# Performance work log

Measured on AMD Instinct MI355X. Metric: run time of the kernel, lower is better.

The kernel has to match this reference:

```python
import jax, jax.numpy as jnp
import numpy as np

DIM = 512
HEADS = 16
HD = DIM // HEADS            # head_dim = 32
WH, WW = 8, 8                # window_size
D0, D1 = 2, 2                # dilated_size
TWH, TWW = WH * D0, WW * D1  # total_window_size = 16,16
SCALE = HD ** -0.5


def _wpart(x, wh, ww):
    # (B,H,W,C) -> (B * H/wh * W/ww, wh, ww, C)
    B, H, W, C = x.shape
    x = x.reshape(B, H // wh, wh, W // ww, ww, C)
    return x.transpose(0, 1, 3, 2, 4, 5).reshape(-1, wh, ww, C)


def _wrev(win, wh, ww, H, W):
    # (nW*B, wh, ww, C) -> (B, H, W, C)
    C = win.shape[-1]
    B = win.shape[0] // ((H // wh) * (W // ww))
    x = win.reshape(B, H // wh, W // ww, wh, ww, C).transpose(0, 1, 3, 2, 4, 5)
    return x.reshape(B, H, W, C)


def _rope2(x):
    # 2D RoPE over a (B, WH, WW, HD) window: first half of HD rotated by row
    # position, second half by column position (axial rotary embedding).
    d = HD // 2
    inv = 1.0 / (10000.0 ** (jnp.arange(0, d, 2, dtype=jnp.float32) / d))  # (d/2,)

    def rot(xp, ang):
        x1, x2 = xp[..., 0::2], xp[..., 1::2]
        c, s = jnp.cos(ang), jnp.sin(ang)
        return jnp.stack([x1 * c - x2 * s, x1 * s + x2 * c], axis=-1).reshape(xp.shape)

    ah = (jnp.arange(WH, dtype=jnp.float32)[:, None] * inv)[:, None, :]  # (WH,1,d/2)
    aw = (jnp.arange(WW, dtype=jnp.float32)[:, None] * inv)[None, :, :]  # (1,WW,d/2)
    return jnp.concatenate([rot(x[..., :d], ah), rot(x[..., d:], aw)], axis=-1)


def _forward(x, qkv_w, qkv_b, proj_w, proj_b):
    B, H, W, C = x.shape
    # partition into total windows, then dilated regrouping
    xw = _wpart(x, TWH, TWW)                                   # (B_, 16, 16, C)
    B_ = xw.shape[0]
    xw = _wpart(xw, D0, D1)                                    # (B_*64, 2, 2, C)
    xw = xw.reshape(B_, WH * WW, D0 * D1, C)
    xw = xw.transpose(0, 2, 1, 3).reshape(B_ * D0 * D1, WH * WW, C)  # (B__, N, C)
    B__, N = xw.shape[0], xw.shape[1]

    qkv = (xw @ qkv_w.T + qkv_b).reshape(B__, N, 3, HEADS, HD).transpose(2, 0, 3, 1, 4)
    q, k, v = qkv[0], qkv[1], qkv[2]                           # (B__, HEADS, N, HD)

    q = _rope2(q.reshape(-1, WH, WW, HD)).reshape(B__, HEADS, N, HD) * SCALE
    k = _rope2(k.reshape(-1, WH, WW, HD)).reshape(B__, HEADS, N, HD)

    attn = jax.nn.softmax(jnp.einsum('bhnd,bhmd->bhnm', q, k), axis=-1)
    out = jnp.einsum('bhnm,bhmd->bhnd', attn, v)               # (B__, HEADS, N, HD)
    out = out.transpose(0, 2, 1, 3).reshape(B__, N, C)

    # undo dilated regrouping, then undo total-window partition
    out = out.reshape(B_, D0 * D1, N, C).transpose(0, 2, 1, 3).reshape(-1, D0, D1, C)
    out = _wrev(out, D0, D1, TWH, TWW)                         # (B_, 16, 16, C)
    out = _wrev(out, TWH, TWW, H, W)                           # (B, H, W, C)
    return out @ proj_w.T + proj_b


def setup_inputs() -> dict:
    key = jax.random.key(0)
    k0, k1, k2 = jax.random.split(key, 3)
    x = jax.random.normal(k0, (4, 128, 128, DIM), dtype=jnp.float32)
    qkv_w = jax.random.normal(k1, (3 * DIM, DIM), dtype=jnp.float32) * (DIM ** -0.5)
    qkv_b = jnp.zeros((3 * DIM,), dtype=jnp.float32)
    proj_w = jax.random.normal(k2, (DIM, DIM), dtype=jnp.float32) * (DIM ** -0.5)
    proj_b = jnp.zeros((DIM,), dtype=jnp.float32)
    return {"x": x, "qkv_w": qkv_w, "qkv_b": qkv_b, "proj_w": proj_w, "proj_b": proj_b}


def reference(x, qkv_w, qkv_b, proj_w, proj_b):
    return _forward(x, qkv_w, qkv_b, proj_w, proj_b)
```

## Files before the change

### kernel.cpp

```cpp
#include <hip/hip_runtime.h>
#include <hip/hip_bf16.h>
#include <stdint.h>

#define DIMC  512
#define NHEAD 16
#define HDIM  32
#define NTOK  65536
#define QKVN  1536
static constexpr float SCALE_F = 0.17677669529663687f;

typedef __attribute__((ext_vector_type(4))) float  f32x4;
typedef __attribute__((ext_vector_type(8))) __bf16 bf16x8;

__device__ __forceinline__ uint16_t f2bf(float f) {
  union { float f; uint32_t u; } v; v.f = f;
  return (uint16_t)((v.u + 0x7FFFu + ((v.u >> 16) & 1u)) >> 16);
}

__device__ __forceinline__ void gload_lds16(const void* g, void* l) {
  __builtin_amdgcn_global_load_lds((const __attribute__((address_space(1))) void*)g,
                                   (__attribute__((address_space(3))) void*)l,
                                   16, 0, 0);
}

__global__ void cvt_f32_bf16(const float* __restrict__ src,
                             uint16_t* __restrict__ dst, int n4)
{
  int i = blockIdx.x * blockDim.x + threadIdx.x;
  const int stride = gridDim.x * blockDim.x;
  for (; i < n4; i += stride) {
    const float4 v = ((const float4*)src)[i];
    ushort4 o;
    o.x = f2bf(v.x); o.y = f2bf(v.y); o.z = f2bf(v.z); o.w = f2bf(v.w);
    ((ushort4*)dst)[i] = o;
  }
}

template <bool OUT_F32>
__global__ __launch_bounds__(512, 2)
void gemm256_8ph(const uint16_t* __restrict__ A,
                 const uint16_t* __restrict__ B,
                 const float* __restrict__ bias,
                 void* __restrict__ Cv,
                 int M, int N, int K, int gx)
{
  __shared__ __align__(16) char lds[131072];

  const int tid = threadIdx.x;
  const int l  = tid & 63, w = tid >> 6;
  const int wm = w >> 2,  wn = w & 3;
  const int lm = l & 15,  lq = l >> 4;

  const int nwg = gridDim.x;
  const int qq = nwg >> 3, rr = nwg & 7;
  const int xcd = blockIdx.x & 7, loc = blockIdx.x >> 3;
  const int sw = (xcd < rr ? xcd * (qq + 1) : rr * (qq + 1) + (xcd - rr) * qq) + loc;
  const long m0 = (long)(sw / gx) * 256;
  const long n0 = (long)(sw % gx) * 256;

  const int srow  = tid >> 3;
  const int scolb = (((tid & 7) ^ (srow & 7)) << 4);
  const uint16_t* Ags = A + (m0 + srow) * (long)K + (scolb >> 1);
  const uint16_t* Bgs = B + (n0 + srow) * (long)K + (scolb >> 1);
  char* ldsW = lds + (w << 10);

#define STAGE(Gs, regionOff, half, kt)                                        \
  {                                                                           \
    const uint16_t* s0_ = (Gs) + (size_t)((half) * 128) * K + (kt);           \
    gload_lds16(s0_,                  ldsW + (regionOff));                    \
    gload_lds16(s0_ + (size_t)64 * K, ldsW + (regionOff) + 8192);             \
  }

  const int colx0 = ((lq ^ (lm & 7)) << 4);
  const int aoff0 = (wm * 64 + lm) * 128 + colx0;
  const int aoff1 = (wm * 64 + lm) * 128 + (colx0 ^ 64);
  const int boff0 = (wn * 32 + lm) * 128 + colx0;
  const int boff1 = (wn * 32 + lm) * 128 + (colx0 ^ 64);

  f32x4  acc[2][2][4][2] = {};
  bf16x8 aX[4][2], aY[4][2];
  bf16x8 b0[2][2], b1[2][2];

#define RD_A(DST, OFF)                                                        \
  _Pragma("unroll") for (int i = 0; i < 4; ++i) {                             \
    DST[i][0] = *(const bf16x8*)(lds + (OFF) + aoff0 + i * 2048);             \
    DST[i][1] = *(const bf16x8*)(lds + (OFF) + aoff1 + i * 2048);             \
  }
#define RD_B(DST, OFF)                                                        \
  _Pragma("unroll") for (int j = 0; j < 2; ++j) {                             \
    DST[j][0] = *(const bf16x8*)(lds + (OFF) + boff0 + j * 2048);             \
    DST[j][1] = *(const bf16x8*)(lds + (OFF) + boff1 + j * 2048);             \
  }
#define MFMA16(AS, BS, QM, QN)                                                \
  __builtin_amdgcn_s_setprio(1);                                              \
  _Pragma("unroll") for (int kk = 0; kk < 2; ++kk)                            \
    _Pragma("unroll") for (int i = 0; i < 4; ++i)                             \
      _Pragma("unroll") for (int j = 0; j < 2; ++j)                           \
        acc[QM][QN][i][j] = __builtin_amdgcn_mfma_f32_16x16x32_bf16(          \
            AS[i][kk], BS[j][kk], acc[QM][QN][i][j], 0, 0, 0);                \
  __builtin_amdgcn_s_setprio(0);
#define VMW(N) asm volatile("s_waitcnt vmcnt(" #N ")");
#define BAR()  __builtin_amdgcn_s_barrier();

  STAGE(Ags, 0,             0, 0)
  STAGE(Bgs, 32768,         0, 0)
  STAGE(Ags, 16384,         1, 0)
  STAGE(Bgs, 49152,         1, 0)
  STAGE(Ags, 65536,         0, 64)
  STAGE(Bgs, 65536 + 32768, 0, 64)
  VMW(8) BAR()
  RD_A(aX, 0) RD_B(b0, 32768)
  VMW(4) BAR()

  for (int t2 = 0; t2 < K / 64; t2 += 2) {
    const int k1 = (t2 + 1) * 64;
    int k2 = (t2 + 2) * 64; if (k2 >= K) k2 = 0;
    int k3 = (t2 + 3) * 64; if (k3 >= K) k3 = 0;

    RD_B(b1, 49152)                 STAGE(Ags, 65536 + 16384, 1, k1)
    MFMA16(aX, b0, 0, 0)            BAR()
    RD_A(aY, 16384)                 STAGE(Bgs, 65536 + 49152, 1, k1)
    MFMA16(aX, b1, 0, 1)            BAR()
    STAGE(Ags, 0, 0, k2)
    MFMA16(aY, b0, 1, 0)            VMW(6) BAR()
    RD_A(aX, 65536) RD_B(b0, 65536 + 32768)
    STAGE(Bgs, 32768, 0, k2)
    MFMA16(aY, b1, 1, 1)            VMW(4) BAR()
    RD_B(b1, 65536 + 49152)         STAGE(Ags, 16384, 1, k2)
    MFMA16(aX, b0, 0, 0)            BAR()
    RD_A(aY, 65536 + 16384)         STAGE(Bgs, 49152, 1, k2)
    MFMA16(aX, b1, 0, 1)            BAR()
    STAGE(Ags, 65536, 0, k3)
    MFMA16(aY, b0, 1, 0)            VMW(6) BAR()
    RD_A(aX, 0) RD_B(b0, 32768)
    STAGE(Bgs, 65536 + 32768, 0, k3)
    MFMA16(aY, b1, 1, 1)            VMW(4) BAR()
  }
#undef STAGE
#undef RD_A
#undef RD_B
#undef MFMA16
#undef VMW
#undef BAR

#pragma unroll
  for (int qm = 0; qm < 2; ++qm)
#pragma unroll
  for (int qn = 0; qn < 2; ++qn)
#pragma unroll
  for (int i = 0; i < 4; ++i)
#pragma unroll
  for (int j = 0; j < 2; ++j) {
    const long m = m0 + qm * 128 + wm * 64 + i * 16 + lq * 4;
    const long n = n0 + qn * 128 + wn * 32 + j * 16 + lm;
    const float bv = bias[n];
#pragma unroll
    for (int r = 0; r < 4; ++r) {
      const float val = acc[qm][qn][i][j][r] + bv;
      if (OUT_F32) ((float*)Cv)[(m + r) * (long)N + n] = val;
      else         ((uint16_t*)Cv)[(m + r) * (long)N + n] = f2bf(val);
    }
  }
}

__global__ void attn_win(const uint16_t* __restrict__ QKV,
                         uint16_t* __restrict__ O)
{
  __shared__ __align__(16) __bf16 Pl[4][64][72];

  const int tid = threadIdx.x;
  const int l  = tid & 63, w = tid >> 6;
  const int lm = l & 15,  lq = l >> 4;
  const int bid = blockIdx.x;
  const int g = bid >> 2;
  const int h = (bid & 3) * 4 + w;

  const int d1 = g & 1, d0 = (g >> 1) & 1;
  const int wx = (g >> 2) & 7, wy = (g >> 5) & 7, bb = g >> 8;
  const long tbase = ((long)(bb * 128 + wy * 16 + d0) * 128) + wx * 16 + d1;

  f32x4 invs;
#pragma unroll
  for (int i = 0; i < 4; ++i)
    invs[i] = exp2f(-1.6609640474436813f * (float)((lq & 1) * 4 + i));

  const int co_q = h * HDIM;
  const int co_k = DIMC + h * HDIM;
  const int co_v = 2 * DIMC + h * HDIM;

  bf16x8 qf[4], kf[4];
#pragma unroll
  for (int f = 0; f < 4; ++f) {
    const int n  = f * 16 + lm;
    const int iy = n >> 3, ix = n & 7;
    const float pos = (lq < 2) ? (float)iy : (float)ix;
    const long t = tbase + iy * 256 + ix * 2;
    const uint16_t* qp = QKV + t * QKVN + co_q + lq * 8;
    const uint16_t* kp = QKV + t * QKVN + co_k + lq * 8;
    {
      bf16x8 raw = *(const bf16x8*)qp, o;
#pragma unroll
      for (int i = 0; i < 4; ++i) {
        float x1 = (float)raw[2 * i], x2 = (float)raw[2 * i + 1];
        float s, c; __sincosf(pos * invs[i], &s, &c);
        o[2 * i]     = (__bf16)((x1 * c - x2 * s) * SCALE_F);
        o[2 * i + 1] = (__bf16)((x1 * s + x2 * c) * SCALE_F);
      }
      qf[f] = o;
    }
    {
      bf16x8 raw = *(const bf16x8*)kp, o;
#pragma unroll
      for (int i = 0; i < 4; ++i) {
        float x1 = (float)raw[2 * i], x2 = (float)raw[2 * i + 1];
        float s, c; __sincosf(pos * invs[i], &s, &c);
        o[2 * i]     = (__bf16)(x1 * c - x2 * s);
        o[2 * i + 1] = (__bf16)(x1 * s + x2 * c);
      }
      kf[f] = o;
    }
  }

  const f32x4 fzero = {0.f, 0.f, 0.f, 0.f};
  f32x4 s[4][4];
#pragma unroll
  for (int mi = 0; mi < 4; ++mi)
#pragma unroll
    for (int ni = 0; ni < 4; ++ni)
      s[mi][ni] = __builtin_amdgcn_mfma_f32_16x16x32_bf16(qf[mi], kf[ni], fzero, 0, 0, 0);

  float rsum[4][4];
#pragma unroll
  for (int mi = 0; mi < 4; ++mi)
#pragma unroll
    for (int r = 0; r < 4; ++r) {
      float m = s[mi][0][r];
#pragma unroll
      for (int ni = 1; ni < 4; ++ni) m = fmaxf(m, s[mi][ni][r]);
      m = fmaxf(m, __shfl_xor(m, 1));
      m = fmaxf(m, __shfl_xor(m, 2));
      m = fmaxf(m, __shfl_xor(m, 4));
      m = fmaxf(m, __shfl_xor(m, 8));
      float sum = 0.f;
#pragma unroll
      for (int ni = 0; ni < 4; ++ni) {
        float p = expf(s[mi][ni][r] - m);
        s[mi][ni][r] = p;
        sum += p;
      }
      sum += __shfl_xor(sum, 1);
      sum += __shfl_xor(sum, 2);
      sum += __shfl_xor(sum, 4);
      sum += __shfl_xor(sum, 8);
      rsum[mi][r] = sum;
    }

#pragma unroll
  for (int mi = 0; mi < 4; ++mi)
#pragma unroll
    for (int ni = 0; ni < 4; ++ni)
#pragma unroll
      for (int r = 0; r < 4; ++r)
        Pl[w][mi * 16 + lq * 4 + r][ni * 16 + lm] = (__bf16)s[mi][ni][r];

  bf16x8 pa[4][2];
#pragma unroll
  for (int mi = 0; mi < 4; ++mi)
#pragma unroll
    for (int kk = 0; kk < 2; ++kk)
      pa[mi][kk] = *(const bf16x8*)(&Pl[w][mi * 16 + lm][kk * 32 + lq * 8]);

  bf16x8 vf[2][2];
#pragma unroll
  for (int kk = 0; kk < 2; ++kk)
#pragma unroll
    for (int n2 = 0; n2 < 2; ++n2) {
      const int nb = kk * 32 + lq * 8;
      const long tb2 = tbase + (long)(nb >> 3) * 256;
      const uint16_t* vp = QKV + co_v + n2 * 16 + lm;
      bf16x8 o;
#pragma unroll
      for (int i = 0; i < 8; ++i)
        o[i] = *(const __bf16*)(vp + (tb2 + 2 * i) * QKVN);
      vf[kk][n2] = o;
    }

  f32x4 oacc[4][2] = {};
#pragma unroll
  for (int kk = 0; kk < 2; ++kk)
#pragma unroll
    for (int mi = 0; mi < 4; ++mi)
#pragma unroll
      for (int n2 = 0; n2 < 2; ++n2)
        oacc[mi][n2] = __builtin_amdgcn_mfma_f32_16x16x32_bf16(
            pa[mi][kk], vf[kk][n2], oacc[mi][n2], 0, 0, 0);

#pragma unroll
  for (int mi = 0; mi < 4; ++mi)
#pragma unroll
    for (int r = 0; r < 4; ++r) {
      const int n = mi * 16 + lq * 4 + r;
      const long t = tbase + (n >> 3) * 256 + (n & 7) * 2;
      const float rinv = 1.0f / rsum[mi][r];
#pragma unroll
      for (int n2 = 0; n2 < 2; ++n2)
        O[t * DIMC + h * HDIM + n2 * 16 + lm] = f2bf(oacc[mi][n2][r] * rinv);
    }
}

extern "C" void kernel_launch(void* const* d_in, const int* in_sizes, int n_in,
                              void* d_out, int out_size, void* d_ws, size_t ws_size,
                              hipStream_t stream)
{
  const float* x      = (const float*)d_in[0];
  const float* qkv_w  = (const float*)d_in[1];
  const float* qkv_b  = (const float*)d_in[2];
  const float* proj_w = (const float*)d_in[3];
  const float* proj_b = (const float*)d_in[4];
  float* out = (float*)d_out;

  uint16_t* xb    = (uint16_t*)d_ws;
  uint16_t* qwb   = xb    + (size_t)NTOK * DIMC;
  uint16_t* pwb   = qwb   + (size_t)QKVN * DIMC;
  uint16_t* qkv   = pwb   + (size_t)DIMC * DIMC;
  uint16_t* attn  = qkv   + (size_t)NTOK * QKVN;

  cvt_f32_bf16<<<2048, 256, 0, stream>>>(x,      xb,  NTOK * DIMC / 4);
  cvt_f32_bf16<<<512,  256, 0, stream>>>(qkv_w,  qwb, QKVN * DIMC / 4);
  cvt_f32_bf16<<<256,  256, 0, stream>>>(proj_w, pwb, DIMC * DIMC / 4);

  gemm256_8ph<false><<<dim3((NTOK / 256) * (QKVN / 256)), dim3(512), 0, stream>>>(
      xb, qwb, qkv_b, qkv, NTOK, QKVN, DIMC, QKVN / 256);

  attn_win<<<dim3(1024 * 4), dim3(256), 0, stream>>>(qkv, attn);

  gemm256_8ph<true><<<dim3((NTOK / 256) * (DIMC / 256)), dim3(512), 0, stream>>>(
      attn, pwb, proj_b, out, NTOK, DIMC, DIMC, DIMC / 256);
}
```

Measured before the change: 297.2 us.

## Fuse QKV projection with windowed attention in one kernel per window

```diff
diff --git a/kernel.cpp b/kernel.cpp
--- a/kernel.cpp
+++ b/kernel.cpp
@@ -33,6 +33,200 @@
     ushort4 o;
     o.x = f2bf(v.x); o.y = f2bf(v.y); o.z = f2bf(v.z); o.w = f2bf(v.w);
     ((ushort4*)dst)[i] = o;
+  }
+}
+
+__global__ __launch_bounds__(512, 1)
+void fused_qkv_attn(const float* __restrict__ x,
+                    const uint16_t* __restrict__ Wq,
+                    const float* __restrict__ qkv_b,
+                    uint16_t* __restrict__ O)
+{
+  __shared__ __align__(16) __bf16 xs[64][512];
+  __shared__ __align__(16) __bf16 scr[8][64][72];
+
+  const int tid = threadIdx.x;
+  const int l  = tid & 63, w = tid >> 6;
+  const int lm = l & 15,  lq = l >> 4;
+  const int g = blockIdx.x;
+  const int d1 = g & 1, d0 = (g >> 1) & 1;
+  const int wx = (g >> 2) & 7, wy = (g >> 5) & 7, bb = g >> 8;
+  const long tbase = ((long)(bb * 128 + wy * 16 + d0) * 128) + wx * 16 + d1;
+
+  char* xsC = (char*)&xs[0][0];
+
+#pragma unroll
+  for (int pass = 0; pass < 8; ++pass) {
+    const int G = pass * 512 + tid;
+    const int row = G >> 6, u = G & 63;
+    const long t = tbase + (row >> 3) * 256 + (row & 7) * 2;
+    const float* src = x + t * DIMC + u * 8;
+    const f32x4 v0 = *(const f32x4*)src;
+    const f32x4 v1 = *(const f32x4*)(src + 4);
+    bf16x8 o;
+#pragma unroll
+    for (int q = 0; q < 4; ++q) { o[q] = (__bf16)v0[q]; o[q + 4] = (__bf16)v1[q]; }
+    *(bf16x8*)(xsC + row * 1024 + ((u ^ (row & 7)) << 4)) = o;
+  }
+  __syncthreads();
+
+  __bf16 (*Sw)[72] = scr[w];
+
+  f32x4 invs;
+#pragma unroll
+  for (int i = 0; i < 4; ++i)
+    invs[i] = exp2f(-1.6609640474436813f * (float)((lq & 1) * 4 + i));
+
+  const f32x4 fzero = {0.f, 0.f, 0.f, 0.f};
+
+  auto gemm_to_scr = [&](int wrow0) {
+    f32x4 acc[4][2] = {};
+    const uint16_t* Wp = Wq + (size_t)wrow0 * DIMC;
+#pragma unroll
+    for (int st = 0; st < 16; ++st) {
+      bf16x8 b[2], a[4];
+#pragma unroll
+      for (int j = 0; j < 2; ++j)
+        b[j] = *(const bf16x8*)(Wp + (size_t)(j * 16 + lm) * DIMC + st * 32 + lq * 8);
+#pragma unroll
+      for (int i = 0; i < 4; ++i)
+        a[i] = *(const bf16x8*)(xsC + (i * 16 + lm) * 1024 +
+                                (((st * 4 + lq) ^ (lm & 7)) << 4));
+#pragma unroll
+      for (int i = 0; i < 4; ++i)
+#pragma unroll
+        for (int j = 0; j < 2; ++j)
+          acc[i][j] = __builtin_amdgcn_mfma_f32_16x16x32_bf16(
+              a[i], b[j], acc[i][j], 0, 0, 0);
+    }
+    const float b0 = qkv_b[wrow0 + lm];
+    const float b1 = qkv_b[wrow0 + 16 + lm];
+#pragma unroll
+    for (int mi = 0; mi < 4; ++mi)
+#pragma unroll
+      for (int r = 0; r < 4; ++r) {
+        Sw[mi * 16 + lq * 4 + r][lm]      = (__bf16)(acc[mi][0][r] + b0);
+        Sw[mi * 16 + lq * 4 + r][16 + lm] = (__bf16)(acc[mi][1][r] + b1);
+      }
+  };
+
+  for (int hp = 0; hp < 2; ++hp) {
+    const int h = w * 2 + hp;
+
+    gemm_to_scr(h * HDIM);
+    bf16x8 qf[4], kf[4];
+#pragma unroll
+    for (int f = 0; f < 4; ++f) {
+      const int n = f * 16 + lm, iy = n >> 3, ix = n & 7;
+      const float pos = (lq < 2) ? (float)iy : (float)ix;
+      bf16x8 raw = *(const bf16x8*)&Sw[n][lq * 8], o;
+#pragma unroll
+      for (int i = 0; i < 4; ++i) {
+        float x1 = (float)raw[2 * i], x2 = (float)raw[2 * i + 1];
+        float s_, c_; __sincosf(pos * invs[i], &s_, &c_);
+        o[2 * i]     = (__bf16)((x1 * c_ - x2 * s_) * SCALE_F);
+        o[2 * i + 1] = (__bf16)((x1 * s_ + x2 * c_) * SCALE_F);
+      }
+      qf[f] = o;
+    }
+    gemm_to_scr(DIMC + h * HDIM);
+#pragma unroll
+    for (int f = 0; f < 4; ++f) {
+      const int n = f * 16 + lm, iy = n >> 3, ix = n & 7;
+      const float pos = (lq < 2) ? (float)iy : (float)ix;
+      bf16x8 raw = *(const bf16x8*)&Sw[n][lq * 8], o;
+#pragma unroll
+      for (int i = 0; i < 4; ++i) {
+        float x1 = (float)raw[2 * i], x2 = (float)raw[2 * i + 1];
+        float s_, c_; __sincosf(pos * invs[i], &s_, &c_);
+        o[2 * i]     = (__bf16)(x1 * c_ - x2 * s_);
+        o[2 * i + 1] = (__bf16)(x1 * s_ + x2 * c_);
+      }
+      kf[f] = o;
+    }
+    gemm_to_scr(2 * DIMC + h * HDIM);
+    bf16x8 vf[2][2];
+#pragma unroll
+    for (int kk = 0; kk < 2; ++kk)
+#pragma unroll
+      for (int n2 = 0; n2 < 2; ++n2) {
+        bf16x8 o;
+#pragma unroll
+        for (int i = 0; i < 8; ++i)
+          o[i] = Sw[kk * 32 + lq * 8 + i][n2 * 16 + lm];
+        vf[kk][n2] = o;
+      }
+
+    f32x4 s[4][4];
+#pragma unroll
+    for (int mi = 0; mi < 4; ++mi)
+#pragma unroll
+      for (int ni = 0; ni < 4; ++ni)
+        s[mi][ni] = __builtin_amdgcn_mfma_f32_16x16x32_bf16(
+            qf[mi], kf[ni], fzero, 0, 0, 0);
+
+    float rsum[4][4];
+#pragma unroll
+    for (int mi = 0; mi < 4; ++mi)
+#pragma unroll
+      for (int r = 0; r < 4; ++r) {
+        float m = s[mi][0][r];
+#pragma unroll
+        for (int ni = 1; ni < 4; ++ni) m = fmaxf(m, s[mi][ni][r]);
+        m = fmaxf(m, __shfl_xor(m, 1));
+        m = fmaxf(m, __shfl_xor(m, 2));
+        m = fmaxf(m, __shfl_xor(m, 4));
+        m = fmaxf(m, __shfl_xor(m, 8));
+        float sum = 0.f;
+#pragma unroll
+        for (int ni = 0; ni < 4; ++ni) {
+          float p = expf(s[mi][ni][r] - m);
+          s[mi][ni][r] = p;
+          sum += p;
+        }
+        sum += __shfl_xor(sum, 1);
+        sum += __shfl_xor(sum, 2);
+        sum += __shfl_xor(sum, 4);
+        sum += __shfl_xor(sum, 8);
+        rsum[mi][r] = sum;
+      }
+
+#pragma unroll
+    for (int mi = 0; mi < 4; ++mi)
+#pragma unroll
+      for (int ni = 0; ni < 4; ++ni)
+#pragma unroll
+        for (int r = 0; r < 4; ++r)
+          Sw[mi * 16 + lq * 4 + r][ni * 16 + lm] = (__bf16)s[mi][ni][r];
+
+    bf16x8 pa[4][2];
+#pragma unroll
+    for (int mi = 0; mi < 4; ++mi)
+#pragma unroll
+      for (int kk = 0; kk < 2; ++kk)
+        pa[mi][kk] = *(const bf16x8*)(&Sw[mi * 16 + lm][kk * 32 + lq * 8]);
+
+    f32x4 oacc[4][2] = {};
+#pragma unroll
+    for (int kk = 0; kk < 2; ++kk)
+#pragma unroll
+      for (int mi = 0; mi < 4; ++mi)
+#pragma unroll
+        for (int n2 = 0; n2 < 2; ++n2)
+          oacc[mi][n2] = __builtin_amdgcn_mfma_f32_16x16x32_bf16(
+              pa[mi][kk], vf[kk][n2], oacc[mi][n2], 0, 0, 0);
+
+#pragma unroll
+    for (int mi = 0; mi < 4; ++mi)
+#pragma unroll
+      for (int r = 0; r < 4; ++r) {
+        const int n = mi * 16 + lq * 4 + r;
+        const long t = tbase + (n >> 3) * 256 + (n & 7) * 2;
+        const float rinv = 1.0f / rsum[mi][r];
+#pragma unroll
+        for (int n2 = 0; n2 < 2; ++n2)
+          O[t * DIMC + h * HDIM + n2 * 16 + lm] = f2bf(oacc[mi][n2][r] * rinv);
+      }
   }
 }
 
@@ -163,151 +357,6 @@
   }
 }
 
-__global__ void attn_win(const uint16_t* __restrict__ QKV,
-                         uint16_t* __restrict__ O)
-{
-  __shared__ __align__(16) __bf16 Pl[4][64][72];
-
-  const int tid = threadIdx.x;
-  const int l  = tid & 63, w = tid >> 6;
-  const int lm = l & 15,  lq = l >> 4;
-  const int bid = blockIdx.x;
-  const int g = bid >> 2;
-  const int h = (bid & 3) * 4 + w;
-
-  const int d1 = g & 1, d0 = (g >> 1) & 1;
-  const int wx = (g >> 2) & 7, wy = (g >> 5) & 7, bb = g >> 8;
-  const long tbase = ((long)(bb * 128 + wy * 16 + d0) * 128) + wx * 16 + d1;
-
-  f32x4 invs;
-#pragma unroll
-  for (int i = 0; i < 4; ++i)
-    invs[i] = exp2f(-1.6609640474436813f * (float)((lq & 1) * 4 + i));
-
-  const int co_q = h * HDIM;
-  const int co_k = DIMC + h * HDIM;
-  const int co_v = 2 * DIMC + h * HDIM;
-
-  bf16x8 qf[4], kf[4];
-#pragma unroll
-  for (int f = 0; f < 4; ++f) {
-    const int n  = f * 16 + lm;
-    const int iy = n >> 3, ix = n & 7;
-    const float pos = (lq < 2) ? (float)iy : (float)ix;
-    const long t = tbase + iy * 256 + ix * 2;
-    const uint16_t* qp = QKV + t * QKVN + co_q + lq * 8;
-    const uint16_t* kp = QKV + t * QKVN + co_k + lq * 8;
-    {
-      bf16x8 raw = *(const bf16x8*)qp, o;
-#pragma unroll
-      for (int i = 0; i < 4; ++i) {
-        float x1 = (float)raw[2 * i], x2 = (float)raw[2 * i + 1];
-        float s, c; __sincosf(pos * invs[i], &s, &c);
-        o[2 * i]     = (__bf16)((x1 * c - x2 * s) * SCALE_F);
-        o[2 * i + 1] = (__bf16)((x1 * s + x2 * c) * SCALE_F);
-      }
-      qf[f] = o;
-    }
-    {
-      bf16x8 raw = *(const bf16x8*)kp, o;
-#pragma unroll
-      for (int i = 0; i < 4; ++i) {
-        float x1 = (float)raw[2 * i], x2 = (float)raw[2 * i + 1];
-        float s, c; __sincosf(pos * invs[i], &s, &c);
-        o[2 * i]     = (__bf16)(x1 * c - x2 * s);
-        o[2 * i + 1] = (__bf16)(x1 * s + x2 * c);
-      }
-      kf[f] = o;
-    }
-  }
-
-  const f32x4 fzero = {0.f, 0.f, 0.f, 0.f};
-  f32x4 s[4][4];
-#pragma unroll
-  for (int mi = 0; mi < 4; ++mi)
-#pragma unroll
-    for (int ni = 0; ni < 4; ++ni)
-      s[mi][ni] = __builtin_amdgcn_mfma_f32_16x16x32_bf16(qf[mi], kf[ni], fzero, 0, 0, 0);
-
-  float rsum[4][4];
-#pragma unroll
-  for (int mi = 0; mi < 4; ++mi)
-#pragma unroll
-    for (int r = 0; r < 4; ++r) {
-      float m = s[mi][0][r];
-#pragma unroll
-      for (int ni = 1; ni < 4; ++ni) m = fmaxf(m, s[mi][ni][r]);
-      m = fmaxf(m, __shfl_xor(m, 1));
-      m = fmaxf(m, __shfl_xor(m, 2));
-      m = fmaxf(m, __shfl_xor(m, 4));
-      m = fmaxf(m, __shfl_xor(m, 8));
-      float sum = 0.f;
-#pragma unroll
-      for (int ni = 0; ni < 4; ++ni) {
-        float p = expf(s[mi][ni][r] - m);
-        s[mi][ni][r] = p;
-        sum += p;
-      }
-      sum += __shfl_xor(sum, 1);
-      sum += __shfl_xor(sum, 2);
-      sum += __shfl_xor(sum, 4);
-      sum += __shfl_xor(sum, 8);
-      rsum[mi][r] = sum;
-    }
-
-#pragma unroll
-  for (int mi = 0; mi < 4; ++mi)
-#pragma unroll
-    for (int ni = 0; ni < 4; ++ni)
-#pragma unroll
-      for (int r = 0; r < 4; ++r)
-        Pl[w][mi * 16 + lq * 4 + r][ni * 16 + lm] = (__bf16)s[mi][ni][r];
-
-  bf16x8 pa[4][2];
-#pragma unroll
-  for (int mi = 0; mi < 4; ++mi)
-#pragma unroll
-    for (int kk = 0; kk < 2; ++kk)
-      pa[mi][kk] = *(const bf16x8*)(&Pl[w][mi * 16 + lm][kk * 32 + lq * 8]);
-
-  bf16x8 vf[2][2];
-#pragma unroll
-  for (int kk = 0; kk < 2; ++kk)
-#pragma unroll
-    for (int n2 = 0; n2 < 2; ++n2) {
-      const int nb = kk * 32 + lq * 8;
-      const long tb2 = tbase + (long)(nb >> 3) * 256;
-      const uint16_t* vp = QKV + co_v + n2 * 16 + lm;
-      bf16x8 o;
-#pragma unroll
-      for (int i = 0; i < 8; ++i)
-        o[i] = *(const __bf16*)(vp + (tb2 + 2 * i) * QKVN);
-      vf[kk][n2] = o;
-    }
-
-  f32x4 oacc[4][2] = {};
-#pragma unroll
-  for (int kk = 0; kk < 2; ++kk)
-#pragma unroll
-    for (int mi = 0; mi < 4; ++mi)
-#pragma unroll
-      for (int n2 = 0; n2 < 2; ++n2)
-        oacc[mi][n2] = __builtin_amdgcn_mfma_f32_16x16x32_bf16(
-            pa[mi][kk], vf[kk][n2], oacc[mi][n2], 0, 0, 0);
-
-#pragma unroll
-  for (int mi = 0; mi < 4; ++mi)
-#pragma unroll
-    for (int r = 0; r < 4; ++r) {
-      const int n = mi * 16 + lq * 4 + r;
-      const long t = tbase + (n >> 3) * 256 + (n & 7) * 2;
-      const float rinv = 1.0f / rsum[mi][r];
-#pragma unroll
-      for (int n2 = 0; n2 < 2; ++n2)
-        O[t * DIMC + h * HDIM + n2 * 16 + lm] = f2bf(oacc[mi][n2][r] * rinv);
-    }
-}
-
 extern "C" void kernel_launch(void* const* d_in, const int* in_sizes, int n_in,
                               void* d_out, int out_size, void* d_ws, size_t ws_size,
                               hipStream_t stream)
@@ -319,20 +368,14 @@
   const float* proj_b = (const float*)d_in[4];
   float* out = (float*)d_out;
 
-  uint16_t* xb    = (uint16_t*)d_ws;
-  uint16_t* qwb   = xb    + (size_t)NTOK * DIMC;
-  uint16_t* pwb   = qwb   + (size_t)QKVN * DIMC;
-  uint16_t* qkv   = pwb   + (size_t)DIMC * DIMC;
-  uint16_t* attn  = qkv   + (size_t)NTOK * QKVN;
-
-  cvt_f32_bf16<<<2048, 256, 0, stream>>>(x,      xb,  NTOK * DIMC / 4);
-  cvt_f32_bf16<<<512,  256, 0, stream>>>(qkv_w,  qwb, QKVN * DIMC / 4);
-  cvt_f32_bf16<<<256,  256, 0, stream>>>(proj_w, pwb, DIMC * DIMC / 4);
-
-  gemm256_8ph<false><<<dim3((NTOK / 256) * (QKVN / 256)), dim3(512), 0, stream>>>(
-      xb, qwb, qkv_b, qkv, NTOK, QKVN, DIMC, QKVN / 256);
-
-  attn_win<<<dim3(1024 * 4), dim3(256), 0, stream>>>(qkv, attn);
+  uint16_t* qwb  = (uint16_t*)d_ws;
+  uint16_t* pwb  = qwb + (size_t)QKVN * DIMC;
+  uint16_t* attn = pwb + (size_t)DIMC * DIMC;
+
+  cvt_f32_bf16<<<512, 256, 0, stream>>>(qkv_w,  qwb, QKVN * DIMC / 4);
+  cvt_f32_bf16<<<256, 256, 0, stream>>>(proj_w, pwb, DIMC * DIMC / 4);
+
+  fused_qkv_attn<<<dim3(1024), dim3(512), 0, stream>>>(x, qwb, qkv_b, attn);
 
   gemm256_8ph<true><<<dim3((NTOK / 256) * (DIMC / 256)), dim3(512), 0, stream>>>(
       attn, pwb, proj_b, out, NTOK, DIMC, DIMC, DIMC / 256);
```

New measurement: 399.6 us. 1.34x slower.

## Fuse windowed attention with output projection GEMM in one kernel

Applied to the files above, without the earlier changes.

```diff
diff --git a/kernel.cpp b/kernel.cpp
--- a/kernel.cpp
+++ b/kernel.cpp
@@ -163,148 +163,209 @@
   }
 }
 
-__global__ void attn_win(const uint16_t* __restrict__ QKV,
-                         uint16_t* __restrict__ O)
+__global__ __launch_bounds__(512, 2)
+void attn_proj(const uint16_t* __restrict__ QKV,
+               const uint16_t* __restrict__ Wp,
+               const float* __restrict__ proj_b,
+               float* __restrict__ out)
 {
-  __shared__ __align__(16) __bf16 Pl[4][64][72];
+  __shared__ __align__(16) __bf16 Sout[64][512];
+  __shared__ __align__(16) char   un[65536];
 
   const int tid = threadIdx.x;
   const int l  = tid & 63, w = tid >> 6;
   const int lm = l & 15,  lq = l >> 4;
-  const int bid = blockIdx.x;
-  const int g = bid >> 2;
-  const int h = (bid & 3) * 4 + w;
-
+  const int g = blockIdx.x;
   const int d1 = g & 1, d0 = (g >> 1) & 1;
   const int wx = (g >> 2) & 7, wy = (g >> 5) & 7, bb = g >> 8;
   const long tbase = ((long)(bb * 128 + wy * 16 + d0) * 128) + wx * 16 + d1;
 
+  char* SoutC = (char*)&Sout[0][0];
+  char* PlC   = un + w * 8192;
+
   f32x4 invs;
 #pragma unroll
   for (int i = 0; i < 4; ++i)
     invs[i] = exp2f(-1.6609640474436813f * (float)((lq & 1) * 4 + i));
 
-  const int co_q = h * HDIM;
-  const int co_k = DIMC + h * HDIM;
-  const int co_v = 2 * DIMC + h * HDIM;
-
-  bf16x8 qf[4], kf[4];
-#pragma unroll
-  for (int f = 0; f < 4; ++f) {
-    const int n  = f * 16 + lm;
-    const int iy = n >> 3, ix = n & 7;
-    const float pos = (lq < 2) ? (float)iy : (float)ix;
-    const long t = tbase + iy * 256 + ix * 2;
-    const uint16_t* qp = QKV + t * QKVN + co_q + lq * 8;
-    const uint16_t* kp = QKV + t * QKVN + co_k + lq * 8;
-    {
-      bf16x8 raw = *(const bf16x8*)qp, o;
-#pragma unroll
-      for (int i = 0; i < 4; ++i) {
-        float x1 = (float)raw[2 * i], x2 = (float)raw[2 * i + 1];
-        float s, c; __sincosf(pos * invs[i], &s, &c);
-        o[2 * i]     = (__bf16)((x1 * c - x2 * s) * SCALE_F);
-        o[2 * i + 1] = (__bf16)((x1 * s + x2 * c) * SCALE_F);
-      }
-      qf[f] = o;
+  const f32x4 fzero = {0.f, 0.f, 0.f, 0.f};
+
+  for (int hp = 0; hp < 2; ++hp) {
+    const int h = w * 2 + hp;
+    const int co_q = h * HDIM;
+    const int co_k = DIMC + h * HDIM;
+    const int co_v = 2 * DIMC + h * HDIM;
+
+    bf16x8 qf[4], kf[4];
+#pragma unroll
+    for (int f = 0; f < 4; ++f) {
+      const int n = f * 16 + lm, iy = n >> 3, ix = n & 7;
+      const float pos = (lq < 2) ? (float)iy : (float)ix;
+      const long t = tbase + iy * 256 + ix * 2;
+      const uint16_t* qp = QKV + t * QKVN + co_q + lq * 8;
+      const uint16_t* kp = QKV + t * QKVN + co_k + lq * 8;
+      {
+        bf16x8 raw = *(const bf16x8*)qp, o;
+#pragma unroll
+        for (int i = 0; i < 4; ++i) {
+          float x1 = (float)raw[2 * i], x2 = (float)raw[2 * i + 1];
+          float s_, c_; __sincosf(pos * invs[i], &s_, &c_);
+          o[2 * i]     = (__bf16)((x1 * c_ - x2 * s_) * SCALE_F);
+          o[2 * i + 1] = (__bf16)((x1 * s_ + x2 * c_) * SCALE_F);
+        }
+        qf[f] = o;
+      }
+      {
+        bf16x8 raw = *(const bf16x8*)kp, o;
+#pragma unroll
+        for (int i = 0; i < 4; ++i) {
+          float x1 = (float)raw[2 * i], x2 = (float)raw[2 * i + 1];
+          float s_, c_; __sincosf(pos * invs[i], &s_, &c_);
+          o[2 * i]     = (__bf16)(x1 * c_ - x2 * s_);
+          o[2 * i + 1] = (__bf16)(x1 * s_ + x2 * c_);
+        }
+        kf[f] = o;
+      }
     }
-    {
-      bf16x8 raw = *(const bf16x8*)kp, o;
-#pragma unroll
-      for (int i = 0; i < 4; ++i) {
-        float x1 = (float)raw[2 * i], x2 = (float)raw[2 * i + 1];
-        float s, c; __sincosf(pos * invs[i], &s, &c);
-        o[2 * i]     = (__bf16)(x1 * c - x2 * s);
-        o[2 * i + 1] = (__bf16)(x1 * s + x2 * c);
-      }
-      kf[f] = o;
+    bf16x8 vf[2][2];
+#pragma unroll
+    for (int kk = 0; kk < 2; ++kk)
+#pragma unroll
+      for (int n2 = 0; n2 < 2; ++n2) {
+        const int nb = kk * 32 + lq * 8;
+        const long tb2 = tbase + (long)(nb >> 3) * 256;
+        const uint16_t* vp = QKV + co_v + n2 * 16 + lm;
+        bf16x8 o;
+#pragma unroll
+        for (int i = 0; i < 8; ++i)
+          o[i] = *(const __bf16*)(vp + (tb2 + 2 * i) * QKVN);
+        vf[kk][n2] = o;
+      }
+
+    f32x4 s[4][4];
+#pragma unroll
+    for (int mi = 0; mi < 4; ++mi)
+#pragma unroll
+      for (int ni = 0; ni < 4; ++ni)
+        s[mi][ni] = __builtin_amdgcn_mfma_f32_16x16x32_bf16(
+            qf[mi], kf[ni], fzero, 0, 0, 0);
+
+    float rsum[4][4];
+#pragma unroll
+    for (int mi = 0; mi < 4; ++mi)
+#pragma unroll
+      for (int r = 0; r < 4; ++r) {
+        float m = s[mi][0][r];
+#pragma unroll
+        for (int ni = 1; ni < 4; ++ni) m = fmaxf(m, s[mi][ni][r]);
+        m = fmaxf(m, __shfl_xor(m, 1));
+        m = fmaxf(m, __shfl_xor(m, 2));
+        m = fmaxf(m, __shfl_xor(m, 4));
+        m = fmaxf(m, __shfl_xor(m, 8));
+        float sum = 0.f;
+#pragma unroll
+        for (int ni = 0; ni < 4; ++ni) {
+          float p = expf(s[mi][ni][r] - m);
+          s[mi][ni][r] = p;
+          sum += p;
+        }
+        sum += __shfl_xor(sum, 1);
+        sum += __shfl_xor(sum, 2);
+        sum += __shfl_xor(sum, 4);
+        sum += __shfl_xor(sum, 8);
+        rsum[mi][r] = sum;
+      }
+
+#pragma unroll
+    for (int mi = 0; mi < 4; ++mi)
+#pragma unroll
+      for (int ni = 0; ni < 4; ++ni)
+#pragma unroll
+        for (int r = 0; r < 4; ++r) {
+          const int row = mi * 16 + lq * 4 + r;
+          const int u   = ni * 2 + (lm >> 3);
+          *(__bf16*)(PlC + row * 128 + ((u ^ (row & 7)) << 4) + (lm & 7) * 2)
+              = (__bf16)s[mi][ni][r];
+        }
+    bf16x8 pa[4][2];
+#pragma unroll
+    for (int mi = 0; mi < 4; ++mi)
+#pragma unroll
+      for (int kk = 0; kk < 2; ++kk)
+        pa[mi][kk] = *(const bf16x8*)(PlC + (mi * 16 + lm) * 128 +
+                                      (((kk * 4 + lq) ^ (lm & 7)) << 4));
+
+    f32x4 oacc[4][2] = {};
+#pragma unroll
+    for (int kk = 0; kk < 2; ++kk)
+#pragma unroll
+      for (int mi = 0; mi < 4; ++mi)
+#pragma unroll
+        for (int n2 = 0; n2 < 2; ++n2)
+          oacc[mi][n2] = __builtin_amdgcn_mfma_f32_16x16x32_bf16(
+              pa[mi][kk], vf[kk][n2], oacc[mi][n2], 0, 0, 0);
+
+#pragma unroll
+    for (int mi = 0; mi < 4; ++mi)
+#pragma unroll
+      for (int r = 0; r < 4; ++r) {
+        const int n = mi * 16 + lq * 4 + r;
+        const float rinv = 1.0f / rsum[mi][r];
+#pragma unroll
+        for (int n2 = 0; n2 < 2; ++n2) {
+          const int u = h * 4 + n2 * 2 + (lm >> 3);
+          *(__bf16*)(SoutC + n * 1024 + ((u ^ (n & 7)) << 4) + (lm & 7) * 2)
+              = (__bf16)(oacc[mi][n2][r] * rinv);
+        }
+      }
+  }
+  __syncthreads();
+
+  const int sr = w * 8 + (l >> 3);
+  const int su = (l & 7) ^ ((l >> 3) & 7);
+  char* unW = un + (w << 10);
+
+  f32x4 acc[4][4] = {};
+  for (int kt = 0; kt < 8; ++kt) {
+#pragma unroll
+    for (int c = 0; c < 8; ++c)
+      gload_lds16(Wp + (size_t)(c * 64 + sr) * DIMC + kt * 64 + su * 8,
+                  unW + c * 8192);
+    __syncthreads();
+
+#pragma unroll
+    for (int kk = 0; kk < 2; ++kk) {
+      bf16x8 a[4], b[4];
+#pragma unroll
+      for (int i = 0; i < 4; ++i)
+        a[i] = *(const bf16x8*)(SoutC + (i * 16 + lm) * 1024 +
+                                ((kt * 8 + ((kk * 4 + lq) ^ (lm & 7))) << 4));
+#pragma unroll
+      for (int j = 0; j < 4; ++j)
+        b[j] = *(const bf16x8*)(un + (w * 64 + j * 16 + lm) * 128 +
+                                (((kk * 4 + lq) ^ (lm & 7)) << 4));
+#pragma unroll
+      for (int i = 0; i < 4; ++i)
+#pragma unroll
+        for (int j = 0; j < 4; ++j)
+          acc[i][j] = __builtin_amdgcn_mfma_f32_16x16x32_bf16(
+              a[i], b[j], acc[i][j], 0, 0, 0);
     }
-  }
-
-  const f32x4 fzero = {0.f, 0.f, 0.f, 0.f};
-  f32x4 s[4][4];
-#pragma unroll
-  for (int mi = 0; mi < 4; ++mi)
-#pragma unroll
-    for (int ni = 0; ni < 4; ++ni)
-      s[mi][ni] = __builtin_amdgcn_mfma_f32_16x16x32_bf16(qf[mi], kf[ni], fzero, 0, 0, 0);
-
-  float rsum[4][4];
-#pragma unroll
-  for (int mi = 0; mi < 4; ++mi)
-#pragma unroll
-    for (int r = 0; r < 4; ++r) {
-      float m = s[mi][0][r];
-#pragma unroll
-      for (int ni = 1; ni < 4; ++ni) m = fmaxf(m, s[mi][ni][r]);
-      m = fmaxf(m, __shfl_xor(m, 1));
-      m = fmaxf(m, __shfl_xor(m, 2));
-      m = fmaxf(m, __shfl_xor(m, 4));
-      m = fmaxf(m, __shfl_xor(m, 8));
-      float sum = 0.f;
-#pragma unroll
-      for (int ni = 0; ni < 4; ++ni) {
-        float p = expf(s[mi][ni][r] - m);
-        s[mi][ni][r] = p;
-        sum += p;
-      }
-      sum += __shfl_xor(sum, 1);
-      sum += __shfl_xor(sum, 2);
-      sum += __shfl_xor(sum, 4);
-      sum += __shfl_xor(sum, 8);
-      rsum[mi][r] = sum;
-    }
-
-#pragma unroll
-  for (int mi = 0; mi < 4; ++mi)
-#pragma unroll
-    for (int ni = 0; ni < 4; ++ni)
-#pragma unroll
-      for (int r = 0; r < 4; ++r)
-        Pl[w][mi * 16 + lq * 4 + r][ni * 16 + lm] = (__bf16)s[mi][ni][r];
-
-  bf16x8 pa[4][2];
-#pragma unroll
-  for (int mi = 0; mi < 4; ++mi)
-#pragma unroll
-    for (int kk = 0; kk < 2; ++kk)
-      pa[mi][kk] = *(const bf16x8*)(&Pl[w][mi * 16 + lm][kk * 32 + lq * 8]);
-
-  bf16x8 vf[2][2];
-#pragma unroll
-  for (int kk = 0; kk < 2; ++kk)
-#pragma unroll
-    for (int n2 = 0; n2 < 2; ++n2) {
-      const int nb = kk * 32 + lq * 8;
-      const long tb2 = tbase + (long)(nb >> 3) * 256;
-      const uint16_t* vp = QKV + co_v + n2 * 16 + lm;
-      bf16x8 o;
-#pragma unroll
-      for (int i = 0; i < 8; ++i)
-        o[i] = *(const __bf16*)(vp + (tb2 + 2 * i) * QKVN);
-      vf[kk][n2] = o;
-    }
-
-  f32x4 oacc[4][2] = {};
-#pragma unroll
-  for (int kk = 0; kk < 2; ++kk)
-#pragma unroll
-    for (int mi = 0; mi < 4; ++mi)
-#pragma unroll
-      for (int n2 = 0; n2 < 2; ++n2)
-        oacc[mi][n2] = __builtin_amdgcn_mfma_f32_16x16x32_bf16(
-            pa[mi][kk], vf[kk][n2], oacc[mi][n2], 0, 0, 0);
-
-#pragma unroll
-  for (int mi = 0; mi < 4; ++mi)
-#pragma unroll
-    for (int r = 0; r < 4; ++r) {
-      const int n = mi * 16 + lq * 4 + r;
-      const long t = tbase + (n >> 3) * 256 + (n & 7) * 2;
-      const float rinv = 1.0f / rsum[mi][r];
-#pragma unroll
-      for (int n2 = 0; n2 < 2; ++n2)
-        O[t * DIMC + h * HDIM + n2 * 16 + lm] = f2bf(oacc[mi][n2][r] * rinv);
+    __syncthreads();
+  }
+
+#pragma unroll
+  for (int i = 0; i < 4; ++i)
+#pragma unroll
+    for (int j = 0; j < 4; ++j) {
+      const int o = w * 64 + j * 16 + lm;
+      const float bv = proj_b[o];
+#pragma unroll
+      for (int r = 0; r < 4; ++r) {
+        const int n = i * 16 + lq * 4 + r;
+        const long t = tbase + (n >> 3) * 256 + (n & 7) * 2;
+        out[t * DIMC + o] = acc[i][j][r] + bv;
+      }
     }
 }
 
@@ -319,11 +380,10 @@
   const float* proj_b = (const float*)d_in[4];
   float* out = (float*)d_out;
 
-  uint16_t* xb    = (uint16_t*)d_ws;
-  uint16_t* qwb   = xb    + (size_t)NTOK * DIMC;
-  uint16_t* pwb   = qwb   + (size_t)QKVN * DIMC;
-  uint16_t* qkv   = pwb   + (size_t)DIMC * DIMC;
-  uint16_t* attn  = qkv   + (size_t)NTOK * QKVN;
+  uint16_t* xb   = (uint16_t*)d_ws;
+  uint16_t* qwb  = xb  + (size_t)NTOK * DIMC;
+  uint16_t* pwb  = qwb + (size_t)QKVN * DIMC;
+  uint16_t* qkv  = pwb + (size_t)DIMC * DIMC;
 
   cvt_f32_bf16<<<2048, 256, 0, stream>>>(x,      xb,  NTOK * DIMC / 4);
   cvt_f32_bf16<<<512,  256, 0, stream>>>(qkv_w,  qwb, QKVN * DIMC / 4);
@@ -332,8 +392,5 @@
   gemm256_8ph<false><<<dim3((NTOK / 256) * (QKVN / 256)), dim3(512), 0, stream>>>(
       xb, qwb, qkv_b, qkv, NTOK, QKVN, DIMC, QKVN / 256);
 
-  attn_win<<<dim3(1024 * 4), dim3(256), 0, stream>>>(qkv, attn);
-
-  gemm256_8ph<true><<<dim3((NTOK / 256) * (DIMC / 256)), dim3(512), 0, stream>>>(
-      attn, pwb, proj_b, out, NTOK, DIMC, DIMC, DIMC / 256);
-}
+  attn_proj<<<dim3(1024), dim3(512), 0, stream>>>(qkv, pwb, proj_b, out);
+}
```

Measured after the change: 471.0 us. 58.5% more time.

## Fuse fp32-to-bf16 input conversion into QKV GEMM A-operand loading

Applied to the files above, without the earlier changes.

```diff
diff --git a/kernel.cpp b/kernel.cpp
--- a/kernel.cpp
+++ b/kernel.cpp
@@ -23,16 +23,177 @@
                                    16, 0, 0);
 }
 
-__global__ void cvt_f32_bf16(const float* __restrict__ src,
-                             uint16_t* __restrict__ dst, int n4)
+__global__ void cvt_weights(const float* __restrict__ qw,
+                            const float* __restrict__ pw,
+                            uint16_t* __restrict__ qd,
+                            uint16_t* __restrict__ pd)
 {
+  const int n4q = QKVN * DIMC / 4;
+  const int n4t = n4q + DIMC * DIMC / 4;
   int i = blockIdx.x * blockDim.x + threadIdx.x;
   const int stride = gridDim.x * blockDim.x;
-  for (; i < n4; i += stride) {
-    const float4 v = ((const float4*)src)[i];
+  for (; i < n4t; i += stride) {
+    const float4 v = (i < n4q) ? ((const float4*)qw)[i] : ((const float4*)pw)[i - n4q];
     ushort4 o;
     o.x = f2bf(v.x); o.y = f2bf(v.y); o.z = f2bf(v.z); o.w = f2bf(v.w);
-    ((ushort4*)dst)[i] = o;
+    if (i < n4q) ((ushort4*)qd)[i] = o; else ((ushort4*)pd)[i - n4q] = o;
+  }
+}
+
+__global__ __launch_bounds__(512, 2)
+void gemm256_qkv(const float* __restrict__ A,
+                 const uint16_t* __restrict__ B,
+                 const float* __restrict__ bias,
+                 uint16_t* __restrict__ C,
+                 int M, int N, int K, int gx)
+{
+  __shared__ __align__(16) char lds[131072];
+
+  const int tid = threadIdx.x;
+  const int l  = tid & 63, w = tid >> 6;
+  const int wm = w >> 2,  wn = w & 3;
+  const int lm = l & 15,  lq = l >> 4;
+
+  const int nwg = gridDim.x;
+  const int qq = nwg >> 3, rr = nwg & 7;
+  const int xcd = blockIdx.x & 7, loc = blockIdx.x >> 3;
+  const int sw = (xcd < rr ? xcd * (qq + 1) : rr * (qq + 1) + (xcd - rr) * qq) + loc;
+  const long m0 = (long)(sw / gx) * 256;
+  const long n0 = (long)(sw % gx) * 256;
+
+  const int srow = tid >> 3;
+  const int sux  = (tid & 7) ^ (srow & 7);
+  const uint16_t* Bgs = B + (n0 + srow) * (long)K + sux * 8;
+  const float*    Agf = A + (m0 + srow) * (long)K + sux * 8;
+  char* ldsW = lds + (w << 10);
+
+#define STAGEB(regionOff, half, kt)                                           \
+  {                                                                           \
+    const uint16_t* s0_ = Bgs + (size_t)((half) * 128) * K + (kt);            \
+    gload_lds16(s0_,                  ldsW + (regionOff));                    \
+    gload_lds16(s0_ + (size_t)64 * K, ldsW + (regionOff) + 8192);             \
+  }
+#define A_ISSUE(SET, half, kt)                                                \
+  {                                                                           \
+    const float* ap_ = Agf + (size_t)((half) * 128) * K + (kt);               \
+    const float* aq_ = ap_ + (size_t)64 * K;                                  \
+    asm volatile("global_load_dwordx4 %0, %1, off" : "=&v"(SET[0]) : "v"(ap_));     \
+    asm volatile("global_load_dwordx4 %0, %1, off" : "=&v"(SET[1]) : "v"(ap_ + 4)); \
+    asm volatile("global_load_dwordx4 %0, %1, off" : "=&v"(SET[2]) : "v"(aq_));     \
+    asm volatile("global_load_dwordx4 %0, %1, off" : "=&v"(SET[3]) : "v"(aq_ + 4)); \
+  }
+#define A_WRITE(SET, regionOff)                                               \
+  {                                                                           \
+    bf16x8 v0_, v1_;                                                          \
+    _Pragma("unroll") for (int q_ = 0; q_ < 4; ++q_) {                        \
+      v0_[q_] = (__bf16)SET[0][q_]; v0_[q_ + 4] = (__bf16)SET[1][q_];         \
+      v1_[q_] = (__bf16)SET[2][q_]; v1_[q_ + 4] = (__bf16)SET[3][q_];         \
+    }                                                                         \
+    *(bf16x8*)(lds + (regionOff) + tid * 16) = v0_;                           \
+    *(bf16x8*)(lds + (regionOff) + 8192 + tid * 16) = v1_;                    \
+  }
+
+  const int colx0 = ((lq ^ (lm & 7)) << 4);
+  const int aoff0 = (wm * 64 + lm) * 128 + colx0;
+  const int aoff1 = (wm * 64 + lm) * 128 + (colx0 ^ 64);
+  const int boff0 = (wn * 32 + lm) * 128 + colx0;
+  const int boff1 = (wn * 32 + lm) * 128 + (colx0 ^ 64);
+
+  f32x4  acc[2][2][4][2] = {};
+  bf16x8 aX[4][2], aY[4][2];
+  bf16x8 b0[2][2], b1[2][2];
+  f32x4  pfA[4], pfB[4];
+
+#define RD_A(DST, OFF)                                                        \
+  _Pragma("unroll") for (int i = 0; i < 4; ++i) {                             \
+    DST[i][0] = *(const bf16x8*)(lds + (OFF) + aoff0 + i * 2048);             \
+    DST[i][1] = *(const bf16x8*)(lds + (OFF) + aoff1 + i * 2048);             \
+  }
+#define RD_B(DST, OFF)                                                        \
+  _Pragma("unroll") for (int j = 0; j < 2; ++j) {                             \
+    DST[j][0] = *(const bf16x8*)(lds + (OFF) + boff0 + j * 2048);             \
+    DST[j][1] = *(const bf16x8*)(lds + (OFF) + boff1 + j * 2048);             \
+  }
+#define MFMA16(AS, BS, QM, QN)                                                \
+  __builtin_amdgcn_s_setprio(1);                                              \
+  _Pragma("unroll") for (int kk = 0; kk < 2; ++kk)                            \
+    _Pragma("unroll") for (int i = 0; i < 4; ++i)                             \
+      _Pragma("unroll") for (int j = 0; j < 2; ++j)                           \
+        acc[QM][QN][i][j] = __builtin_amdgcn_mfma_f32_16x16x32_bf16(          \
+            AS[i][kk], BS[j][kk], acc[QM][QN][i][j], 0, 0, 0);                \
+  __builtin_amdgcn_s_setprio(0);
+#define VMW(N) asm volatile("s_waitcnt vmcnt(" #N ")");
+#define SB()   __builtin_amdgcn_sched_barrier(0);
+#define BAR()  __builtin_amdgcn_s_barrier();
+
+  A_ISSUE(pfB, 0, 0)
+  STAGEB(32768, 0, 0)
+  STAGEB(49152, 1, 0)
+  VMW(0) SB()
+  A_WRITE(pfB, 0)
+  A_ISSUE(pfB, 1, 0)
+  VMW(0) SB()
+  A_WRITE(pfB, 16384)
+  A_ISSUE(pfB, 0, 64)
+  VMW(0) SB()
+  A_WRITE(pfB, 65536)
+  A_ISSUE(pfA, 1, 64)
+  STAGEB(65536 + 32768, 0, 64)
+  BAR()
+  RD_A(aX, 0) RD_B(b0, 32768)
+
+  for (int t2 = 0; t2 < K / 64; t2 += 2) {
+    const int k1 = (t2 + 1) * 64;
+    int k2 = (t2 + 2) * 64; if (k2 >= K) k2 = 0;
+    int k3 = (t2 + 3) * 64; if (k3 >= K) k3 = 0;
+
+    RD_B(b1, 49152)
+    VMW(2) SB() A_WRITE(pfA, 65536 + 16384) A_ISSUE(pfB, 0, k2)
+    MFMA16(aX, b0, 0, 0)  BAR()
+    RD_A(aY, 16384)
+    STAGEB(65536 + 49152, 1, k1)
+    MFMA16(aX, b1, 0, 1)  BAR()
+    VMW(2) SB() A_WRITE(pfB, 0) A_ISSUE(pfA, 1, k2)
+    MFMA16(aY, b0, 1, 0)  BAR()
+    RD_A(aX, 65536) RD_B(b0, 65536 + 32768)
+    STAGEB(32768, 0, k2)
+    MFMA16(aY, b1, 1, 1)  VMW(6) BAR()
+    RD_B(b1, 65536 + 49152)
+    VMW(2) SB() A_WRITE(pfA, 16384) A_ISSUE(pfB, 0, k3)
+    MFMA16(aX, b0, 0, 0)  BAR()
+    RD_A(aY, 65536 + 16384)
+    STAGEB(49152, 1, k2)
+    MFMA16(aX, b1, 0, 1)  BAR()
+    VMW(2) SB() A_WRITE(pfB, 65536) A_ISSUE(pfA, 1, k3)
+    MFMA16(aY, b0, 1, 0)  BAR()
+    RD_A(aX, 0) RD_B(b0, 32768)
+    STAGEB(65536 + 32768, 0, k3)
+    MFMA16(aY, b1, 1, 1)  VMW(6) BAR()
+  }
+#undef STAGEB
+#undef A_ISSUE
+#undef A_WRITE
+#undef RD_A
+#undef RD_B
+#undef MFMA16
+#undef VMW
+#undef SB
+#undef BAR
+
+#pragma unroll
+  for (int qm = 0; qm < 2; ++qm)
+#pragma unroll
+  for (int qn = 0; qn < 2; ++qn)
+#pragma unroll
+  for (int i = 0; i < 4; ++i)
+#pragma unroll
+  for (int j = 0; j < 2; ++j) {
+    const long m = m0 + qm * 128 + wm * 64 + i * 16 + lq * 4;
+    const long n = n0 + qn * 128 + wn * 32 + j * 16 + lm;
+    const float bv = bias[n];
+#pragma unroll
+    for (int r = 0; r < 4; ++r)
+      C[(m + r) * (long)N + n] = f2bf(acc[qm][qn][i][j][r] + bv);
   }
 }
 
@@ -319,18 +480,15 @@
   const float* proj_b = (const float*)d_in[4];
   float* out = (float*)d_out;
 
-  uint16_t* xb    = (uint16_t*)d_ws;
-  uint16_t* qwb   = xb    + (size_t)NTOK * DIMC;
-  uint16_t* pwb   = qwb   + (size_t)QKVN * DIMC;
-  uint16_t* qkv   = pwb   + (size_t)DIMC * DIMC;
-  uint16_t* attn  = qkv   + (size_t)NTOK * QKVN;
-
-  cvt_f32_bf16<<<2048, 256, 0, stream>>>(x,      xb,  NTOK * DIMC / 4);
-  cvt_f32_bf16<<<512,  256, 0, stream>>>(qkv_w,  qwb, QKVN * DIMC / 4);
-  cvt_f32_bf16<<<256,  256, 0, stream>>>(proj_w, pwb, DIMC * DIMC / 4);
-
-  gemm256_8ph<false><<<dim3((NTOK / 256) * (QKVN / 256)), dim3(512), 0, stream>>>(
-      xb, qwb, qkv_b, qkv, NTOK, QKVN, DIMC, QKVN / 256);
+  uint16_t* qwb  = (uint16_t*)d_ws;
+  uint16_t* pwb  = qwb + (size_t)QKVN * DIMC;
+  uint16_t* qkv  = pwb + (size_t)DIMC * DIMC;
+  uint16_t* attn = qkv + (size_t)NTOK * QKVN;
+
+  cvt_weights<<<768, 256, 0, stream>>>(qkv_w, proj_w, qwb, pwb);
+
+  gemm256_qkv<<<dim3((NTOK / 256) * (QKVN / 256)), dim3(512), 0, stream>>>(
+      x, qwb, qkv_b, qkv, NTOK, QKVN, DIMC, QKVN / 256);
 
   attn_win<<<dim3(1024 * 4), dim3(256), 0, stream>>>(qkv, attn);
 
```

After: 337.0 us. +13.4%, slower.
